# Performance work log

Measured on AMD Instinct MI355X. Metric: run time of the kernel, lower is better.

Reference implementation:

```python
import jax, jax.numpy as jnp
import numpy as np


def mish(x):
    return x * jnp.tanh(jax.nn.softplus(x))


def gcn(x, W, b, src, dst):
    # PyG GCNConv: h = D^-1/2 (A+I) D^-1/2 (x W) + b, aggregation at dst=edge_index[1]
    n = x.shape[0]
    h = x @ W
    deg = jax.ops.segment_sum(jnp.ones(src.shape[0], x.dtype), dst, num_segments=n) + 1.0
    dinv = jax.lax.rsqrt(deg)
    msg = h[src] * (dinv[src] * dinv[dst])[:, None]
    agg = jax.ops.segment_sum(msg, dst, num_segments=n)
    return agg + h * (dinv * dinv)[:, None] + b


def pool_mean(x, seg, num_segments):
    s = jax.ops.segment_sum(x, seg, num_segments=num_segments)
    c = jax.ops.segment_sum(jnp.ones(x.shape[0], x.dtype), seg, num_segments=num_segments)
    return s / jnp.maximum(c, 1.0)[:, None]


def attention(x, qW, qb, kW, kb, vW, vb, G):
    # x: [G*R, in_feats] -> per-graph self-attention over ROIs (dropout is identity in eval)
    R = x.shape[0] // G
    xc = x.reshape(G, R, x.shape[1])
    Q = xc @ qW + qb
    K = xc @ kW + kb
    Vv = xc @ vW + vb
    scores = jnp.einsum('gqd,gkd->gqk', Q, K) / (Q.shape[-1] ** 0.5)
    w = jax.nn.softmax(scores, axis=-1)
    out = jnp.einsum('gqk,gkd->gqd', w, Vv).reshape(G * R, Vv.shape[-1])
    return out, w.mean(axis=0)


def closs(a, b, temp=0.6):
    a = a / jnp.maximum(jnp.linalg.norm(a, axis=1, keepdims=True), 1e-12)
    b = b / jnp.maximum(jnp.linalg.norm(b, axis=1, keepdims=True), 1e-12)
    logits = (a @ b.T) / temp
    return -jnp.mean(jnp.diagonal(jax.nn.log_softmax(logits, axis=1)))


def setup_inputs() -> dict:
    key = jax.random.key(0)
    G, R1, R2, F_IN, H, OUT, DEG, V = 512, 200, 160, 128, 64, 64, 16, 64
    N1, N2 = G * R1, G * R2
    ks = iter(jax.random.split(key, 64))
    d = {}
    d['x1'] = jax.random.normal(next(ks), (N1, R1 + 3), jnp.float32)
    d['x2'] = jax.random.normal(next(ks), (N2, R2 + 3), jnp.float32)

    def lin(name, i, o):
        d[name + '_W'] = jax.random.normal(next(ks), (i, o), jnp.float32) * (i ** -0.5)
        d[name + '_b'] = jnp.zeros((o,), jnp.float32)

    lin('fcl', R1 + 3, F_IN); lin('fcr', R2 + 3, F_IN)
    lin('fcl1', R1, F_IN); lin('fcr1', R2, F_IN)
    lin('a1_q', F_IN, OUT); lin('a1_k', F_IN, OUT); lin('a1_v', F_IN, OUT)
    lin('a2_q', F_IN, OUT); lin('a2_k', F_IN, OUT); lin('a2_v', F_IN, OUT)
    lin('conv', F_IN, H); lin('conv1', H, H)
    lin('mlp', H, OUT)
    lin('fc1a', OUT * 4, F_IN); lin('fc1b', F_IN, 2)

    def edges(k, R):
        k1, k2 = jax.random.split(k)
        off = (jnp.arange(G, dtype=jnp.int32) * R)[:, None]
        src = jax.random.randint(k1, (G, R * DEG), 0, R, jnp.int32) + off
        dst = jax.random.randint(k2, (G, R * DEG), 0, R, jnp.int32) + off
        return jnp.stack([src.reshape(-1), dst.reshape(-1)])

    d['edge_index1'] = edges(next(ks), R1)
    d['edge_index2'] = edges(next(ks), R2)
    d['batch1'] = jnp.repeat(jnp.arange(G, dtype=jnp.int32), R1)
    d['batch2'] = jnp.repeat(jnp.arange(G, dtype=jnp.int32), R2)

    def sub(k, R):
        # one visited-node set (as in RW_subgraph) tiled per graph with offsets
        vis = jnp.sort(jax.random.permutation(k, R)[:V]).astype(jnp.int32)
        return (vis[None, :] + (jnp.arange(G, dtype=jnp.int32) * R)[:, None]).reshape(-1)

    d['sub_idx1'] = sub(next(ks), R1)
    d['sub_idx2'] = sub(next(ks), R2)
    d['num_graphs'] = G
    return d


def reference(x1, x2, fcl_W, fcl_b, fcr_W, fcr_b, fcl1_W, fcl1_b, fcr1_W, fcr1_b,
              a1_q_W, a1_q_b, a1_k_W, a1_k_b, a1_v_W, a1_v_b,
              a2_q_W, a2_q_b, a2_k_W, a2_k_b, a2_v_W, a2_v_b,
              conv_W, conv_b, conv1_W, conv1_b, mlp_W, mlp_b,
              fc1a_W, fc1a_b, fc1b_W, fc1b_b,
              edge_index1, edge_index2, batch1, batch2, sub_idx1, sub_idx2, num_graphs):
    G = int(num_graphs)
    src1, dst1 = edge_index1[0], edge_index1[1]
    src2, dst2 = edge_index2[0], edge_index2[1]

    z1 = x1[:, :-3] @ fcl1_W + fcl1_b
    z2 = x2[:, :-3] @ fcr1_W + fcr1_b
    z1, aw1 = attention(z1, a1_q_W, a1_q_b, a1_k_W, a1_k_b, a1_v_W, a1_v_b, G)
    z2, aw2 = attention(z2, a2_q_W, a2_q_b, a2_k_W, a2_k_b, a2_v_W, a2_v_b, G)
    z1 = pool_mean(z1, batch1, G)
    z2 = pool_mean(z2, batch2, G)

    h1 = x1 @ fcl_W + fcl_b
    h2 = x2 @ fcr_W + fcr_b
    o1 = mish(gcn(h1, conv_W, conv_b, src1, dst1))
    o2 = mish(gcn(h2, conv_W, conv_b, src2, dst2))
    o1 = gcn(o1, conv1_W, conv1_b, src1, dst1)
    o2 = gcn(o2, conv1_W, conv1_b, src2, dst2)

    s1 = o1[sub_idx1] @ mlp_W + mlp_b
    s2 = o2[sub_idx2] @ mlp_W + mlp_b
    s1 = pool_mean(s1, batch1[sub_idx1], G)
    s2 = pool_mean(s2, batch2[sub_idx2], G)

    c_loss = closs(s1, z2) + closs(z1, s2)
    feat = jnp.concatenate([s1, z1, s2, z2], axis=1)
    out = mish(feat @ fc1a_W + fc1a_b) @ fc1b_W + fc1b_b
    return c_loss, out, aw1, aw2
```

## Files before the change

### kernel.cpp

```cpp
#include <hip/hip_runtime.h>
#include <math.h>

#define TPB 256
#define MAXR 200
#define MAXEP 4608

typedef float f32x4 __attribute__((ext_vector_type(4)));
typedef __bf16 bfv8 __attribute__((ext_vector_type(8)));

union U8 { uint4 q; unsigned short us[8]; __bf16 b[8]; bfv8 v; };

__device__ __forceinline__ unsigned short f2bfu(float f) {
  union { __bf16 h; unsigned short u; } x;
  x.h = (__bf16)f;
  return x.u;
}
__device__ __forceinline__ float bfu2f(unsigned short u) {
  return __uint_as_float((unsigned)u << 16);
}

__device__ __forceinline__ float mish_f(float x) {
  float sp = fmaxf(x, 0.f) + log1pf(expf(-fabsf(x)));
  return x * tanhf(sp);
}

__device__ __forceinline__ U8 loadA_f32(const float* Af, int kb, int K, bool rowok) {
  U8 u;
  if (rowok && kb + 8 <= K) {
    float4 f0 = *(const float4*)(Af + kb);
    float4 f1 = *(const float4*)(Af + kb + 4);
    u.b[0]=(__bf16)f0.x; u.b[1]=(__bf16)f0.y; u.b[2]=(__bf16)f0.z; u.b[3]=(__bf16)f0.w;
    u.b[4]=(__bf16)f1.x; u.b[5]=(__bf16)f1.y; u.b[6]=(__bf16)f1.z; u.b[7]=(__bf16)f1.w;
  } else {
#pragma unroll
    for (int j = 0; j < 8; ++j) {
      float f = (rowok && kb + j < K) ? Af[kb + j] : 0.f;
      u.b[j] = (__bf16)f;
    }
  }
  return u;
}

template<bool ABF16, bool CBF16, int NJ, int KPMAX>
__global__ __launch_bounds__(256) void gemm2(
    const void* __restrict__ Av, const unsigned short* __restrict__ Bt,
    const float* __restrict__ bias, void* __restrict__ Cv,
    int N, int M, int K, int lda, int ldc,
    long sA, long sB, long sC, float alpha, int Kpad)
{
  constexpr int BM = NJ * 16;
  __shared__ unsigned short Bs[BM * KPMAX];

  const int tid = threadIdx.x;
  const int col0 = blockIdx.x * BM, row0 = blockIdx.y * 64;

  {
    const unsigned short* Bp = Bt + (long)blockIdx.z * sB + (long)col0 * Kpad;
    int rows = M - col0; if (rows > BM) rows = BM;
    const int total = rows * Kpad;
    for (int i = tid * 8; i < total; i += TPB * 32) {
      uint4 a0, a1, a2, a3;
      bool b1 = i + TPB * 8  < total;
      bool b2 = i + TPB * 16 < total;
      bool b3 = i + TPB * 24 < total;
      a0 = *(const uint4*)&Bp[i];
      if (b1) a1 = *(const uint4*)&Bp[i + TPB * 8];
      if (b2) a2 = *(const uint4*)&Bp[i + TPB * 16];
      if (b3) a3 = *(const uint4*)&Bp[i + TPB * 24];
      *(uint4*)&Bs[i] = a0;
      if (b1) *(uint4*)&Bs[i + TPB * 8]  = a1;
      if (b2) *(uint4*)&Bs[i + TPB * 16] = a2;
      if (b3) *(uint4*)&Bs[i + TPB * 24] = a3;
    }
  }

  const int lane = tid & 63, w = tid >> 6;
  const int mrow = lane & 15, kg = lane >> 4;
  const int arow = row0 + w * 16 + mrow;
  const bool rowok = arow < N;

  const unsigned short* Ah = nullptr;
  const float* Af = nullptr;
  if (ABF16) Ah = (const unsigned short*)Av + (long)blockIdx.z * sA + (long)arow * lda;
  else       Af = (const float*)Av + (long)blockIdx.z * sA + (long)arow * lda;

  U8 ua;
  if (ABF16) ua.q = *(const uint4*)(Ah + kg * 8);
  else       ua   = loadA_f32(Af, kg * 8, K, rowok);

  __syncthreads();

  f32x4 acc[NJ];
#pragma unroll
  for (int j = 0; j < NJ; ++j) acc[j] = (f32x4)0.f;

  for (int k0 = 0; k0 < K; k0 += 32) {
    U8 un;
    bool more = (k0 + 32) < K;
    if (more) {
      if (ABF16) un.q = *(const uint4*)(Ah + k0 + 32 + kg * 8);
      else       un   = loadA_f32(Af, k0 + 32 + kg * 8, K, rowok);
    }
    const int kb = k0 + kg * 8;
#pragma unroll
    for (int j = 0; j < NJ; ++j) {
      U8 ub;
      ub.q = *(const uint4*)&Bs[(j * 16 + mrow) * Kpad + kb];
      acc[j] = __builtin_amdgcn_mfma_f32_16x16x32_bf16(ua.v, ub.v, acc[j], 0, 0, 0);
    }
    if (more) ua = un;
  }

  long cbase = (long)blockIdx.z * sC;
#pragma unroll
  for (int j = 0; j < NJ; ++j) {
    int gc = col0 + j * 16 + mrow;
    if (gc >= M) continue;
    float bb = bias ? bias[gc] : 0.f;
#pragma unroll
    for (int r = 0; r < 4; ++r) {
      int gr = row0 + w * 16 + kg * 4 + r;
      if (gr >= N) continue;
      float v = acc[j][r] * alpha + bb;
      if (CBF16) ((unsigned short*)Cv)[cbase + (long)gr * ldc + gc] = f2bfu(v);
      else       ((float*)Cv)[cbase + (long)gr * ldc + gc] = v;
    }
  }
}

static inline int kpad_of(int K) { return ((K + 31) / 32) * 32 + 8; }

struct PrepSeg { const float* src; void* dst; int K, M, Kpad, kind; };
struct PrepArgs { PrepSeg s[19]; };

__global__ __launch_bounds__(256) void prep_weights(PrepArgs a) {
  PrepSeg sg = a.s[blockIdx.x];
  if (sg.kind == 0) {
    unsigned short* d = (unsigned short*)sg.dst;
    int tot = sg.M * sg.Kpad;
    for (int i = threadIdx.x; i < tot; i += TPB) {
      int m = i / sg.Kpad, k = i - m * sg.Kpad;
      float f = (k < sg.K) ? sg.src[(long)k * sg.M + m] : 0.f;
      d[i] = f2bfu(f);
    }
  } else {
    float* d = (float*)sg.dst;
    for (int i = threadIdx.x; i < sg.K; i += TPB) d[i] = sg.src[i];
  }
}

__global__ __launch_bounds__(256) void xcast(const float* __restrict__ x,
                                             unsigned short* __restrict__ xb,
                                             int C, int S)
{
  long r0 = (long)blockIdx.x * 8;
  for (int i = threadIdx.x; i < 8 * S; i += TPB) {
    int rr = i / S, c = i - rr * S;
    long r = r0 + rr;
    xb[r * S + c] = f2bfu(c < C ? x[r * C + c] : 0.f);
  }
}

__global__ __launch_bounds__(256) void ktvt_kernel(
    const unsigned short* __restrict__ QKV, unsigned short* __restrict__ Kt,
    unsigned short* __restrict__ Vt, int R, int Rpad)
{
  int g = blockIdx.x;
  const unsigned short* q = QKV + (long)g * R * 192;
  unsigned short* kt = Kt + (long)g * R * 72;
  unsigned short* vt = Vt + (long)g * 64 * Rpad;
  int c = threadIdx.x & 63, w = threadIdx.x >> 6;
  for (int r = w; r < R; r += 4) {
    kt[r * 72 + c] = q[(long)r * 192 + 64 + c];
    vt[c * Rpad + r] = q[(long)r * 192 + 128 + c];
  }
  int pad = Rpad - R;
  for (int i = threadIdx.x; i < 64 * pad; i += TPB) {
    int cc = i / pad, k = i - cc * pad;
    vt[cc * Rpad + R + k] = 0;
  }
}

__global__ __launch_bounds__(256) void gcn_kernel(
    const unsigned short* __restrict__ hWb, const int* __restrict__ src,
    const int* __restrict__ dst, const float* __restrict__ bias,
    unsigned short* __restrict__ outb, int R, int EPG, int do_mish)
{
  __shared__ unsigned short hWs[(MAXR + 1) * 64];
  __shared__ float dinv_s[MAXR];
  __shared__ unsigned short ssrc[MAXEP];
  __shared__ int cnt[256];
  __shared__ int scan[256];
  __shared__ int offx[257];
  __shared__ int cur[256];

  int g = blockIdx.x, tid = threadIdx.x;
  long base = (long)g * R * 64;
  long ebase = (long)g * EPG;
  int gR = g * R;
  int RF = R * 64;

  cnt[tid] = 0;
  __syncthreads();
  for (int e = tid; e < EPG; e += TPB)
    atomicAdd(&cnt[dst[ebase + e] - gR], 1);
  __syncthreads();

  int x = cnt[tid];
  int pc = (x + 7) & ~7;
  scan[tid] = pc;
  __syncthreads();
#pragma unroll
  for (int s = 1; s < 256; s <<= 1) {
    int t = (tid >= s) ? scan[tid - s] : 0;
    __syncthreads();
    scan[tid] += t;
    __syncthreads();
  }
  if (tid == 0) offx[0] = 0;
  offx[tid + 1] = scan[tid];
  cur[tid] = scan[tid] - pc;
  if (tid < R) dinv_s[tid] = rsqrtf((float)x + 1.f);
  {
    unsigned dummy2 = (unsigned)R | ((unsigned)R << 16);
    for (int i = tid; i < MAXEP / 2; i += TPB) ((unsigned*)ssrc)[i] = dummy2;
  }
  __syncthreads();

  for (int e = tid; e < EPG; e += TPB) {
    int d = dst[ebase + e] - gR;
    int s = src[ebase + e] - gR;
    int pos = atomicAdd(&cur[d], 1);
    ssrc[pos] = (unsigned short)s;
  }
  for (int i = tid * 8; i < RF; i += TPB * 8) {
    U8 u; u.q = *(const uint4*)&hWb[base + i];
    float di = dinv_s[i >> 6];
#pragma unroll
    for (int j = 0; j < 8; ++j) u.us[j] = f2bfu(bfu2f(u.us[j]) * di);
    *(uint4*)&hWs[i] = u.q;
  }
  if (tid < 64) hWs[(R << 6) | tid] = 0;
  __syncthreads();

  int lane = tid & 63, w = tid >> 6;
  for (int d = w; d < R; d += 4) {
    int i = offx[d], eEnd = offx[d + 1];
    float acc = 0.f;
    for (; i < eEnd; i += 8) {
      U8 u; u.q = *(const uint4*)&ssrc[i];
      float a0 = bfu2f(hWs[((int)u.us[0] << 6) | lane]);
      float a1 = bfu2f(hWs[((int)u.us[1] << 6) | lane]);
      float a2 = bfu2f(hWs[((int)u.us[2] << 6) | lane]);
      float a3 = bfu2f(hWs[((int)u.us[3] << 6) | lane]);
      float a4 = bfu2f(hWs[((int)u.us[4] << 6) | lane]);
      float a5 = bfu2f(hWs[((int)u.us[5] << 6) | lane]);
      float a6 = bfu2f(hWs[((int)u.us[6] << 6) | lane]);
      float a7 = bfu2f(hWs[((int)u.us[7] << 6) | lane]);
      acc += ((a0 + a1) + (a2 + a3)) + ((a4 + a5) + (a6 + a7));
    }
    float di = dinv_s[d];
    float v = di * (acc + bfu2f(hWs[(d << 6) | lane])) + bias[lane];
    if (do_mish) v = mish_f(v);
    outb[base + ((long)d << 6) + lane] = f2bfu(v);
  }
}

__global__ __launch_bounds__(256) void softmax_bf16(unsigned short* __restrict__ S,
                                                    int R, long rows)
{
  long wid = (long)blockIdx.x * 4 + (threadIdx.x >> 6);
  if (wid >= rows) return;
  int lane = threadIdx.x & 63;
  unsigned short* row = S + wid * R;
  float v[4];
  float mx = -1e30f;
#pragma unroll
  for (int t = 0; t < 4; ++t) {
    int j = lane + t * 64;
    v[t] = (j < R) ? bfu2f(row[j]) : -1e30f;
    mx = fmaxf(mx, v[t]);
  }
#pragma unroll
  for (int o = 32; o; o >>= 1) mx = fmaxf(mx, __shfl_xor(mx, o));
  float s = 0.f;
#pragma unroll
  for (int t = 0; t < 4; ++t) {
    int j = lane + t * 64;
    if (j < R) { v[t] = expf(v[t] - mx); s += v[t]; }
  }
#pragma unroll
  for (int o = 32; o; o >>= 1) s += __shfl_xor(s, o);
  float inv = 1.f / s;
#pragma unroll
  for (int t = 0; t < 4; ++t) {
    int j = lane + t * 64;
    if (j < R) row[j] = f2bfu(v[t] * inv);
  }
}

__global__ void meang_bf16(const unsigned short* __restrict__ S, float* __restrict__ out,
                           int RR, int G, float inv)
{
  int idx = blockIdx.x * TPB + threadIdx.x;
  if (idx >= RR) return;
  const unsigned short* p = S + idx;
  float s = 0.f;
  for (int g = 0; g + 8 <= G; g += 8) {
    s += bfu2f(p[(long)g * RR])       + bfu2f(p[(long)(g + 1) * RR]) +
         bfu2f(p[(long)(g + 2) * RR]) + bfu2f(p[(long)(g + 3) * RR]) +
         bfu2f(p[(long)(g + 4) * RR]) + bfu2f(p[(long)(g + 5) * RR]) +
         bfu2f(p[(long)(g + 6) * RR]) + bfu2f(p[(long)(g + 7) * RR]);
  }
  out[idx] = s * inv;
}

__global__ __launch_bounds__(64) void pool_mean_kernel(const float* __restrict__ X,
                                                       float* __restrict__ out, int R)
{
  int g = blockIdx.x, lane = threadIdx.x;
  const float* p = X + (long)g * R * 64 + lane;
  float s = 0.f;
  for (int r = 0; r + 4 <= R; r += 4)
    s += p[(long)r * 64] + p[(long)(r + 1) * 64] + p[(long)(r + 2) * 64] + p[(long)(r + 3) * 64];
  out[g * 64 + lane] = s * (1.f / R);
}

__global__ __launch_bounds__(64) void sub_mean_kernel(const unsigned short* __restrict__ X,
                                                      const int* __restrict__ sub,
                                                      float* __restrict__ out, int V)
{
  int g = blockIdx.x, lane = threadIdx.x;
  float s = 0.f;
  for (int v = 0; v + 4 <= V; v += 4) {
    int i0 = sub[g * V + v],     i1 = sub[g * V + v + 1];
    int i2 = sub[g * V + v + 2], i3 = sub[g * V + v + 3];
    s += bfu2f(X[(long)i0 * 64 + lane]) + bfu2f(X[(long)i1 * 64 + lane]) +
         bfu2f(X[(long)i2 * 64 + lane]) + bfu2f(X[(long)i3 * 64 + lane]);
  }
  out[g * 64 + lane] = s * (1.f / V);
}

__global__ __launch_bounds__(64) void norm_rows_kernel(const float* __restrict__ X,
                                                       float* __restrict__ Y)
{
  int g = blockIdx.x, lane = threadIdx.x;
  float x = X[g * 64 + lane];
  float ss = x * x;
#pragma unroll
  for (int o = 32; o; o >>= 1) ss += __shfl_xor(ss, o);
  float n = fmaxf(sqrtf(ss), 1e-12f);
  Y[g * 64 + lane] = x / n;
}

__global__ __launch_bounds__(256) void closs_kernel(const float* __restrict__ An,
                                                    const float* __restrict__ Bn,
                                                    float* __restrict__ loss, int G,
                                                    float invTemp, float coef)
{
  int i = blockIdx.x;
  __shared__ float arow[64];
  __shared__ float logits[512];
  __shared__ float red[256];
  int t = threadIdx.x;
  if (t < 64) arow[t] = An[i * 64 + t];
  __syncthreads();
  for (int j = t; j < G; j += 256) {
    const float* bp = Bn + (long)j * 64;
    float d = 0.f;
#pragma unroll
    for (int k = 0; k < 64; ++k) d = fmaf(arow[k], bp[k], d);
    logits[j] = d * invTemp;
  }
  __syncthreads();
  float mx = -1e30f;
  for (int j = t; j < G; j += 256) mx = fmaxf(mx, logits[j]);
  red[t] = mx; __syncthreads();
  for (int o = 128; o; o >>= 1) { if (t < o) red[t] = fmaxf(red[t], red[t + o]); __syncthreads(); }
  mx = red[0]; __syncthreads();
  float s = 0.f;
  for (int j = t; j < G; j += 256) s += expf(logits[j] - mx);
  red[t] = s; __syncthreads();
  for (int o = 128; o; o >>= 1) { if (t < o) red[t] += red[t + o]; __syncthreads(); }
  if (t == 0) {
    float lse = mx + logf(red[0]);
    atomicAdd(loss, coef * (lse - logits[i]));
  }
}

__global__ __launch_bounds__(128) void head_kernel(
    const float* __restrict__ s1, const float* __restrict__ z1,
    const float* __restrict__ s2, const float* __restrict__ z2,
    const float* __restrict__ W1, const float* __restrict__ b1,
    const float* __restrict__ W2, const float* __restrict__ b2,
    float* __restrict__ out)
{
  int g = blockIdx.x, t = threadIdx.x;
  __shared__ float feat[256];
  __shared__ float hid[128];
  if (t < 64) {
    feat[t]       = s1[g * 64 + t];
    feat[64 + t]  = z1[g * 64 + t];
    feat[128 + t] = s2[g * 64 + t];
    feat[192 + t] = z2[g * 64 + t];
  }
  __syncthreads();
  float acc = b1[t];
  for (int k = 0; k < 256; ++k) acc = fmaf(feat[k], W1[k * 128 + t], acc);
  hid[t] = mish_f(acc);
  __syncthreads();
  if (t < 2) {
    float a2 = b2[t];
#pragma unroll
    for (int k = 0; k < 128; ++k) a2 = fmaf(hid[k], W2[k * 2 + t], a2);
    out[g * 2 + t] = a2;
  }
}

#define LAUNCH_GEMM(ABF,CBF,NJ,KP, A,B,BI,C, N,M,K,LDA,LDC,SA,SB,SC,BAT,AL,KPAD) \
  { dim3 g_(((M)+(NJ)*16-1)/((NJ)*16), ((N)+63)/64, (BAT)); \
    gemm2<ABF,CBF,NJ,KP><<<g_,256,0,stream>>>((A),(B),(BI),(C),(N),(M),(K),(LDA),(LDC),(SA),(SB),(SC),(AL),(KPAD)); }

extern "C" void kernel_launch(void* const* d_in, const int* in_sizes, int n_in,
                              void* d_out, int out_size, void* d_ws, size_t ws_size,
                              hipStream_t stream)
{
  const float* x1     = (const float*)d_in[0];
  const float* x2     = (const float*)d_in[1];
  const float* fcl_W  = (const float*)d_in[2];  const float* fcl_b  = (const float*)d_in[3];
  const float* fcr_W  = (const float*)d_in[4];  const float* fcr_b  = (const float*)d_in[5];
  const float* fcl1_W = (const float*)d_in[6];  const float* fcl1_b = (const float*)d_in[7];
  const float* fcr1_W = (const float*)d_in[8];  const float* fcr1_b = (const float*)d_in[9];
  const float* a1qW = (const float*)d_in[10]; const float* a1qb = (const float*)d_in[11];
  const float* a1kW = (const float*)d_in[12]; const float* a1kb = (const float*)d_in[13];
  const float* a1vW = (const float*)d_in[14]; const float* a1vb = (const float*)d_in[15];
  const float* a2qW = (const float*)d_in[16]; const float* a2qb = (const float*)d_in[17];
  const float* a2kW = (const float*)d_in[18]; const float* a2kb = (const float*)d_in[19];
  const float* a2vW = (const float*)d_in[20]; const float* a2vb = (const float*)d_in[21];
  const float* convW  = (const float*)d_in[22]; const float* convb  = (const float*)d_in[23];
  const float* conv1W = (const float*)d_in[24]; const float* conv1b = (const float*)d_in[25];
  const float* mlpW   = (const float*)d_in[26]; const float* mlpb   = (const float*)d_in[27];
  const float* fc1aW  = (const float*)d_in[28]; const float* fc1ab  = (const float*)d_in[29];
  const float* fc1bW  = (const float*)d_in[30]; const float* fc1bb  = (const float*)d_in[31];
  const int* ei1  = (const int*)d_in[32];
  const int* ei2  = (const int*)d_in[33];
  const int* sub1 = (const int*)d_in[36];
  const int* sub2 = (const int*)d_in[37];

  const int R1 = in_sizes[6] / 128;
  const int R2 = in_sizes[8] / 128;
  const int N1 = in_sizes[34];
  const int N2 = in_sizes[35];
  const int G  = N1 / R1;
  const int E1 = in_sizes[32] / 2, E2 = in_sizes[33] / 2;
  const int EPG1 = E1 / G, EPG2 = E2 / G;
  const int V = in_sizes[36] / G;

  const int XS = 232;
  const int Kp1  = kpad_of(R1);
  const int Kp2  = kpad_of(R2);
  const int Kp1f = kpad_of(R1 + 3);
  const int Kp2f = kpad_of(R2 + 3);
  const int Rpad1 = Kp1, Rpad2 = Kp2;

  char* wp = (char*)d_ws;
  auto alloc = [&](size_t bytes) -> char* {
    char* p = wp; wp += (bytes + 255) & ~(size_t)255; return p;
  };
  unsigned short* x1b = (unsigned short*)alloc((size_t)N1 * XS * 2);
  unsigned short* x2b = (unsigned short*)alloc((size_t)N2 * XS * 2);
  size_t raSh = (size_t)G * R1 * R1;
  if ((size_t)N1 * 128 > raSh) raSh = (size_t)N1 * 128;
  unsigned short* RA = (unsigned short*)alloc(raSh * 2);
  unsigned short* RB = (unsigned short*)alloc((size_t)N1 * 192 * 2);
  unsigned short* Kt = (unsigned short*)alloc((size_t)G * R1 * 72 * 2);
  unsigned short* Vt = (unsigned short*)alloc((size_t)G * 64 * Rpad1 * 2);
  float* W5 = (float*)alloc((size_t)N1 * 64 * 4);
  unsigned short* fcl1t  = (unsigned short*)alloc((size_t)128 * Kp1 * 2);
  unsigned short* fcr1t  = (unsigned short*)alloc((size_t)128 * Kp2 * 2);
  unsigned short* fclt   = (unsigned short*)alloc((size_t)128 * Kp1f * 2);
  unsigned short* fcrt   = (unsigned short*)alloc((size_t)128 * Kp2f * 2);
  unsigned short* Wc1t   = (unsigned short*)alloc((size_t)192 * 136 * 2);
  unsigned short* Wc2t   = (unsigned short*)alloc((size_t)192 * 136 * 2);
  unsigned short* convt  = (unsigned short*)alloc((size_t)64 * 136 * 2);
  unsigned short* conv1t = (unsigned short*)alloc((size_t)64 * 72 * 2);
  unsigned short* mlpt   = (unsigned short*)alloc((size_t)64 * 72 * 2);
  float* bc1 = (float*)alloc(192 * 4);
  float* bc2 = (float*)alloc(192 * 4);
  float* Pz1 = (float*)alloc((size_t)G * 64 * 4);
  float* Pz2 = (float*)alloc((size_t)G * 64 * 4);
  float* Ps1 = (float*)alloc((size_t)G * 64 * 4);
  float* Ps2 = (float*)alloc((size_t)G * 64 * 4);
  float* Mt  = (float*)alloc((size_t)G * 64 * 4);
  float* n_s1 = (float*)alloc((size_t)G * 64 * 4);
  float* n_z2 = (float*)alloc((size_t)G * 64 * 4);
  float* n_z1 = (float*)alloc((size_t)G * 64 * 4);
  float* n_s2 = (float*)alloc((size_t)G * 64 * 4);
  (void)alloc(4096);

  float* loss = (float*)d_out;
  float* outp = loss + 1;
  float* aw1  = outp + (size_t)G * 2;
  float* aw2  = aw1 + (size_t)R1 * R1;

  hipMemsetAsync(d_out, 0, sizeof(float), stream);

  PrepArgs pa;
  int seg = 0;
  auto addp = [&](const float* s, unsigned short* d, int K, int M, int Kp) {
    pa.s[seg].src = s; pa.s[seg].dst = d; pa.s[seg].K = K; pa.s[seg].M = M;
    pa.s[seg].Kpad = Kp; pa.s[seg].kind = 0; seg++;
  };
  auto addb = [&](const float* s, float* d, int n) {
    pa.s[seg].src = s; pa.s[seg].dst = d; pa.s[seg].K = n; pa.s[seg].M = 0;
    pa.s[seg].Kpad = 0; pa.s[seg].kind = 1; seg++;
  };
  addp(fcl1_W, fcl1t, R1, 128, Kp1);
  addp(fcr1_W, fcr1t, R2, 128, Kp2);
  addp(fcl_W,  fclt,  R1 + 3, 128, Kp1f);
  addp(fcr_W,  fcrt,  R2 + 3, 128, Kp2f);
  addp(a1qW, Wc1t,             128, 64, 136);
  addp(a1kW, Wc1t + 64 * 136,  128, 64, 136);
  addp(a1vW, Wc1t + 128 * 136, 128, 64, 136);
  addp(a2qW, Wc2t,             128, 64, 136);
  addp(a2kW, Wc2t + 64 * 136,  128, 64, 136);
  addp(a2vW, Wc2t + 128 * 136, 128, 64, 136);
  addp(convW,  convt,  128, 64, 136);
  addp(conv1W, conv1t, 64, 64, 72);
  addp(mlpW,   mlpt,   64, 64, 72);
  addb(a1qb, bc1, 64); addb(a1kb, bc1 + 64, 64); addb(a1vb, bc1 + 128, 64);
  addb(a2qb, bc2, 64); addb(a2kb, bc2 + 64, 64); addb(a2vb, bc2 + 128, 64);
  prep_weights<<<seg, 256, 0, stream>>>(pa);

  xcast<<<N1 / 8, 256, 0, stream>>>(x1, x1b, R1 + 3, XS);
  xcast<<<N2 / 8, 256, 0, stream>>>(x2, x2b, R2 + 3, XS);

  LAUNCH_GEMM(true, true, 8, 232, x1b, fcl1t, fcl1_b, RA,
              N1, 128, R1, XS, 128, 0, 0, 0, 1, 1.f, Kp1);
  LAUNCH_GEMM(true, true, 12, 136, RA, Wc1t, bc1, RB,
              N1, 192, 128, 128, 192, 0, 0, 0, 1, 1.f, 136);
  ktvt_kernel<<<G, 256, 0, stream>>>(RB, Kt, Vt, R1, Rpad1);
  LAUNCH_GEMM(true, true, 8, 72, RB, Kt, nullptr, RA,
              R1, R1, 64, 192, R1, (long)R1 * 192, (long)R1 * 72, (long)R1 * R1,
              G, 0.125f, 72);
  {
    long rows = (long)G * R1;
    softmax_bf16<<<(int)((rows + 3) / 4), 256, 0, stream>>>(RA, R1, rows);
    meang_bf16<<<(R1 * R1 + TPB - 1) / TPB, TPB, 0, stream>>>(RA, aw1, R1 * R1, G, 1.f / G);
  }
  LAUNCH_GEMM(true, false, 4, 232, RA, Vt, nullptr, W5,
              R1, 64, R1, R1, 64, (long)R1 * R1, (long)64 * Rpad1, (long)R1 * 64,
              G, 1.f, Rpad1);
  pool_mean_kernel<<<G, 64, 0, stream>>>(W5, Pz1, R1);

  LAUNCH_GEMM(true, true, 8, 232, x2b, fcr1t, fcr1_b, RA,
              N2, 128, R2, XS, 128, 0, 0, 0, 1, 1.f, Kp2);
  LAUNCH_GEMM(true, true, 12, 136, RA, Wc2t, bc2, RB,
              N2, 192, 128, 128, 192, 0, 0, 0, 1, 1.f, 136);
  ktvt_kernel<<<G, 256, 0, stream>>>(RB, Kt, Vt, R2, Rpad2);
  LAUNCH_GEMM(true, true, 8, 72, RB, Kt, nullptr, RA,
              R2, R2, 64, 192, R2, (long)R2 * 192, (long)R2 * 72, (long)R2 * R2,
              G, 0.125f, 72);
  {
    long rows = (long)G * R2;
    softmax_bf16<<<(int)((rows + 3) / 4), 256, 0, stream>>>(RA, R2, rows);
    meang_bf16<<<(R2 * R2 + TPB - 1) / TPB, TPB, 0, stream>>>(RA, aw2, R2 * R2, G, 1.f / G);
  }
  LAUNCH_GEMM(true, false, 4, 232, RA, Vt, nullptr, W5,
              R2, 64, R2, R2, 64, (long)R2 * R2, (long)64 * Rpad2, (long)R2 * 64,
              G, 1.f, Rpad2);
  pool_mean_kernel<<<G, 64, 0, stream>>>(W5, Pz2, R2);

  unsigned short* hW0 = RB;
  unsigned short* hW1 = RB + (size_t)N1 * 64;
  unsigned short* hW2 = RB + (size_t)N1 * 128;
  LAUNCH_GEMM(true, true, 8, 232, x1b, fclt, fcl_b, RA,
              N1, 128, R1 + 3, XS, 128, 0, 0, 0, 1, 1.f, Kp1f);
  LAUNCH_GEMM(true, true, 4, 136, RA, convt, nullptr, hW0,
              N1, 64, 128, 128, 64, 0, 0, 0, 1, 1.f, 136);
  gcn_kernel<<<G, 256, 0, stream>>>(hW0, ei1, ei1 + E1, convb, hW1, R1, EPG1, 1);
  LAUNCH_GEMM(true, true, 4, 136, hW1, conv1t, nullptr, hW2,
              N1, 64, 64, 64, 64, 0, 0, 0, 1, 1.f, 72);
  gcn_kernel<<<G, 256, 0, stream>>>(hW2, ei1, ei1 + E1, conv1b, hW0, R1, EPG1, 0);
  sub_mean_kernel<<<G, 64, 0, stream>>>(hW0, sub1, Mt, V);
  LAUNCH_GEMM(false, false, 4, 136, Mt, mlpt, mlpb, Ps1,
              G, 64, 64, 64, 64, 0, 0, 0, 1, 1.f, 72);

  LAUNCH_GEMM(true, true, 8, 232, x2b, fcrt, fcr_b, RA,
              N2, 128, R2 + 3, XS, 128, 0, 0, 0, 1, 1.f, Kp2f);
  LAUNCH_GEMM(true, true, 4, 136, RA, convt, nullptr, hW0,
              N2, 64, 128, 128, 64, 0, 0, 0, 1, 1.f, 136);
  gcn_kernel<<<G, 256, 0, stream>>>(hW0, ei2, ei2 + E2, convb, hW1, R2, EPG2, 1);
  LAUNCH_GEMM(true, true, 4, 136, hW1, conv1t, nullptr, hW2,
              N2, 64, 64, 64, 64, 0, 0, 0, 1, 1.f, 72);
  gcn_kernel<<<G, 256, 0, stream>>>(hW2, ei2, ei2 + E2, conv1b, hW0, R2, EPG2, 0);
  sub_mean_kernel<<<G, 64, 0, stream>>>(hW0, sub2, Mt, V);
  LAUNCH_GEMM(false, false, 4, 136, Mt, mlpt, mlpb, Ps2,
              G, 64, 64, 64, 64, 0, 0, 0, 1, 1.f, 72);

  norm_rows_kernel<<<G, 64, 0, stream>>>(Ps1, n_s1);
  norm_rows_kernel<<<G, 64, 0, stream>>>(Pz2, n_z2);
  norm_rows_kernel<<<G, 64, 0, stream>>>(Pz1, n_z1);
  norm_rows_kernel<<<G, 64, 0, stream>>>(Ps2, n_s2);
  const float invTemp = 1.f / 0.6f;
  closs_kernel<<<G, 256, 0, stream>>>(n_s1, n_z2, loss, G, invTemp, 1.f / G);
  closs_kernel<<<G, 256, 0, stream>>>(n_z1, n_s2, loss, G, invTemp, 1.f / G);

  head_kernel<<<G, 128, 0, stream>>>(Ps1, Pz1, Ps2, Pz2, fc1aW, fc1ab, fc1bW, fc1bb, outp);
}
```

Baseline: 941.5 us.

## Replace sparse GCN aggregation with dense per-graph normalized adjacency MFMA GEMM

Each graph's normalized adjacency (with self-loops and D^-1/2 scaling) is built once as a dense bf16 matrix, and GCN aggregation becomes a batched MFMA GEMM against the transposed features, with bias and mish fused into the GEMM epilogue. The attention output is also written as bf16, and pool_mean switches to a 256-thread bf16 reduction. This swaps LDS gather aggregation for tensor-core dense work, at the cost of extra adjacency-build and transpose kernels and O(R^2) dense FLOPs on a sparse graph. The adjacency is stored in bf16 and overwrites the x buffers, which adds rounding error.

```diff
diff --git a/kernel.cpp b/kernel.cpp
--- a/kernel.cpp
+++ b/kernel.cpp
@@ -41,7 +41,7 @@
   return u;
 }
 
-template<bool ABF16, bool CBF16, int NJ, int KPMAX>
+template<bool ABF16, bool CBF16, bool MISH, int NJ, int KPMAX>
 __global__ __launch_bounds__(256) void gemm2(
     const void* __restrict__ Av, const unsigned short* __restrict__ Bt,
     const float* __restrict__ bias, void* __restrict__ Cv,
@@ -122,6 +122,7 @@
       int gr = row0 + w * 16 + kg * 4 + r;
       if (gr >= N) continue;
       float v = acc[j][r] * alpha + bb;
+      if (MISH) v = mish_f(v);
       if (CBF16) ((unsigned short*)Cv)[cbase + (long)gr * ldc + gc] = f2bfu(v);
       else       ((float*)Cv)[cbase + (long)gr * ldc + gc] = v;
     }
@@ -181,24 +182,21 @@
   }
 }
 
-__global__ __launch_bounds__(256) void gcn_kernel(
-    const unsigned short* __restrict__ hWb, const int* __restrict__ src,
-    const int* __restrict__ dst, const float* __restrict__ bias,
-    unsigned short* __restrict__ outb, int R, int EPG, int do_mish)
-{
-  __shared__ unsigned short hWs[(MAXR + 1) * 64];
-  __shared__ float dinv_s[MAXR];
+__global__ __launch_bounds__(256) void adj_build(
+    const int* __restrict__ src, const int* __restrict__ dst,
+    unsigned short* __restrict__ Adj, int R, int Rpad, int EPG)
+{
+  __shared__ float dinv_s[256];
   __shared__ unsigned short ssrc[MAXEP];
   __shared__ int cnt[256];
   __shared__ int scan[256];
   __shared__ int offx[257];
   __shared__ int cur[256];
+  __shared__ float rowbuf[4][256];
 
   int g = blockIdx.x, tid = threadIdx.x;
-  long base = (long)g * R * 64;
   long ebase = (long)g * EPG;
   int gR = g * R;
-  int RF = R * 64;
 
   cnt[tid] = 0;
   __syncthreads();
@@ -220,9 +218,9 @@
   if (tid == 0) offx[0] = 0;
   offx[tid + 1] = scan[tid];
   cur[tid] = scan[tid] - pc;
-  if (tid < R) dinv_s[tid] = rsqrtf((float)x + 1.f);
+  dinv_s[tid] = rsqrtf((float)x + 1.f);
   {
-    unsigned dummy2 = (unsigned)R | ((unsigned)R << 16);
+    unsigned dummy2 = 0xFFFFFFFFu;
     for (int i = tid; i < MAXEP / 2; i += TPB) ((unsigned*)ssrc)[i] = dummy2;
   }
   __syncthreads();
@@ -233,36 +231,55 @@
     int pos = atomicAdd(&cur[d], 1);
     ssrc[pos] = (unsigned short)s;
   }
-  for (int i = tid * 8; i < RF; i += TPB * 8) {
-    U8 u; u.q = *(const uint4*)&hWb[base + i];
-    float di = dinv_s[i >> 6];
-#pragma unroll
-    for (int j = 0; j < 8; ++j) u.us[j] = f2bfu(bfu2f(u.us[j]) * di);
-    *(uint4*)&hWs[i] = u.q;
-  }
-  if (tid < 64) hWs[(R << 6) | tid] = 0;
   __syncthreads();
 
   int lane = tid & 63, w = tid >> 6;
+  float* rb = rowbuf[w];
   for (int d = w; d < R; d += 4) {
-    int i = offx[d], eEnd = offx[d + 1];
-    float acc = 0.f;
-    for (; i < eEnd; i += 8) {
-      U8 u; u.q = *(const uint4*)&ssrc[i];
-      float a0 = bfu2f(hWs[((int)u.us[0] << 6) | lane]);
-      float a1 = bfu2f(hWs[((int)u.us[1] << 6) | lane]);
-      float a2 = bfu2f(hWs[((int)u.us[2] << 6) | lane]);
-      float a3 = bfu2f(hWs[((int)u.us[3] << 6) | lane]);
-      float a4 = bfu2f(hWs[((int)u.us[4] << 6) | lane]);
-      float a5 = bfu2f(hWs[((int)u.us[5] << 6) | lane]);
-      float a6 = bfu2f(hWs[((int)u.us[6] << 6) | lane]);
-      float a7 = bfu2f(hWs[((int)u.us[7] << 6) | lane]);
-      acc += ((a0 + a1) + (a2 + a3)) + ((a4 + a5) + (a6 + a7));
-    }
-    float di = dinv_s[d];
-    float v = di * (acc + bfu2f(hWs[(d << 6) | lane])) + bias[lane];
-    if (do_mish) v = mish_f(v);
-    outb[base + ((long)d << 6) + lane] = f2bfu(v);
+#pragma unroll
+    for (int i = 0; i < 4; ++i) rb[lane + i * 64] = 0.f;
+    int i0 = offx[d], i1 = offx[d + 1];
+    for (int i = i0 + lane; i < i1; i += 64) {
+      int s = ssrc[i];
+      if (s < R) atomicAdd(&rb[s], dinv_s[s]);
+    }
+    float dd = dinv_s[d];
+    int c0 = lane * 4;
+    if (c0 < Rpad) {
+      ushort4 o;
+      float v0 = rb[c0]     + (c0     == d ? dd : 0.f);
+      float v1 = rb[c0 + 1] + (c0 + 1 == d ? dd : 0.f);
+      float v2 = rb[c0 + 2] + (c0 + 2 == d ? dd : 0.f);
+      float v3 = rb[c0 + 3] + (c0 + 3 == d ? dd : 0.f);
+      o.x = f2bfu(v0 * dd); o.y = f2bfu(v1 * dd);
+      o.z = f2bfu(v2 * dd); o.w = f2bfu(v3 * dd);
+      *(ushort4*)&Adj[((long)gR + d) * Rpad + c0] = o;
+    }
+  }
+}
+
+__global__ __launch_bounds__(256) void transp64(
+    const unsigned short* __restrict__ X, unsigned short* __restrict__ XT,
+    int R, int Rpad)
+{
+  __shared__ unsigned short tile[64][72];
+  int g = blockIdx.x, tid = threadIdx.x;
+  const unsigned short* xg = X + (long)g * R * 64;
+  unsigned short* xt = XT + (long)g * 64 * Rpad;
+  for (int r0 = 0; r0 < Rpad; r0 += 64) {
+    __syncthreads();
+    for (int i = tid; i < 64 * 64; i += TPB) {
+      int rr = i >> 6, cc = i & 63;
+      int r = r0 + rr;
+      tile[cc][rr] = (r < R) ? xg[(long)r * 64 + cc] : (unsigned short)0;
+    }
+    __syncthreads();
+    int c = tid >> 2, j0 = (tid & 3) * 16;
+    int lim = Rpad - r0; if (lim > 64) lim = 64;
+    for (int jj = j0; jj < j0 + 16 && jj < lim; jj += 8) {
+      uint4 q = *(const uint4*)&tile[c][jj];
+      *(uint4*)&xt[(long)c * Rpad + r0 + jj] = q;
+    }
   }
 }
 
@@ -315,15 +332,18 @@
   out[idx] = s * inv;
 }
 
-__global__ __launch_bounds__(64) void pool_mean_kernel(const float* __restrict__ X,
-                                                       float* __restrict__ out, int R)
-{
-  int g = blockIdx.x, lane = threadIdx.x;
-  const float* p = X + (long)g * R * 64 + lane;
+__global__ __launch_bounds__(256) void pool_mean_bf16(const unsigned short* __restrict__ X,
+                                                      float* __restrict__ out, int R)
+{
+  __shared__ float part[4][64];
+  int g = blockIdx.x, lane = threadIdx.x & 63, w = threadIdx.x >> 6;
   float s = 0.f;
-  for (int r = 0; r + 4 <= R; r += 4)
-    s += p[(long)r * 64] + p[(long)(r + 1) * 64] + p[(long)(r + 2) * 64] + p[(long)(r + 3) * 64];
-  out[g * 64 + lane] = s * (1.f / R);
+  for (int r = w; r < R; r += 4)
+    s += bfu2f(X[((long)g * R + r) * 64 + lane]);
+  part[w][lane] = s;
+  __syncthreads();
+  if (w == 0)
+    out[g * 64 + lane] = (part[0][lane] + part[1][lane] + part[2][lane] + part[3][lane]) * (1.f / R);
 }
 
 __global__ __launch_bounds__(64) void sub_mean_kernel(const unsigned short* __restrict__ X,
@@ -417,9 +437,9 @@
   }
 }
 
-#define LAUNCH_GEMM(ABF,CBF,NJ,KP, A,B,BI,C, N,M,K,LDA,LDC,SA,SB,SC,BAT,AL,KPAD) \
+#define LAUNCH_GEMM(ABF,CBF,MISH,NJ,KP, A,B,BI,C, N,M,K,LDA,LDC,SA,SB,SC,BAT,AL,KPAD) \
   { dim3 g_(((M)+(NJ)*16-1)/((NJ)*16), ((N)+63)/64, (BAT)); \
-    gemm2<ABF,CBF,NJ,KP><<<g_,256,0,stream>>>((A),(B),(BI),(C),(N),(M),(K),(LDA),(LDC),(SA),(SB),(SC),(AL),(KPAD)); }
+    gemm2<ABF,CBF,MISH,NJ,KP><<<g_,256,0,stream>>>((A),(B),(BI),(C),(N),(M),(K),(LDA),(LDC),(SA),(SB),(SC),(AL),(KPAD)); }
 
 extern "C" void kernel_launch(void* const* d_in, const int* in_sizes, int n_in,
                               void* d_out, int out_size, void* d_ws, size_t ws_size,
@@ -475,7 +495,7 @@
   unsigned short* RB = (unsigned short*)alloc((size_t)N1 * 192 * 2);
   unsigned short* Kt = (unsigned short*)alloc((size_t)G * R1 * 72 * 2);
   unsigned short* Vt = (unsigned short*)alloc((size_t)G * 64 * Rpad1 * 2);
-  float* W5 = (float*)alloc((size_t)N1 * 64 * 4);
+  unsigned short* W5 = (unsigned short*)alloc((size_t)N1 * 64 * 2);
   unsigned short* fcl1t  = (unsigned short*)alloc((size_t)128 * Kp1 * 2);
   unsigned short* fcr1t  = (unsigned short*)alloc((size_t)128 * Kp2 * 2);
   unsigned short* fclt   = (unsigned short*)alloc((size_t)128 * Kp1f * 2);
@@ -497,6 +517,9 @@
   float* n_z1 = (float*)alloc((size_t)G * 64 * 4);
   float* n_s2 = (float*)alloc((size_t)G * 64 * 4);
   (void)alloc(4096);
+
+  unsigned short* Adj1 = x1b;
+  unsigned short* Adj2 = x2b;
 
   float* loss = (float*)d_out;
   float* outp = loss + 1;
@@ -535,12 +558,12 @@
   xcast<<<N1 / 8, 256, 0, stream>>>(x1, x1b, R1 + 3, XS);
   xcast<<<N2 / 8, 256, 0, stream>>>(x2, x2b, R2 + 3, XS);
 
-  LAUNCH_GEMM(true, true, 8, 232, x1b, fcl1t, fcl1_b, RA,
+  LAUNCH_GEMM(true, true, false, 8, 232, x1b, fcl1t, fcl1_b, RA,
               N1, 128, R1, XS, 128, 0, 0, 0, 1, 1.f, Kp1);
-  LAUNCH_GEMM(true, true, 12, 136, RA, Wc1t, bc1, RB,
+  LAUNCH_GEMM(true, true, false, 12, 136, RA, Wc1t, bc1, RB,
               N1, 192, 128, 128, 192, 0, 0, 0, 1, 1.f, 136);
   ktvt_kernel<<<G, 256, 0, stream>>>(RB, Kt, Vt, R1, Rpad1);
-  LAUNCH_GEMM(true, true, 8, 72, RB, Kt, nullptr, RA,
+  LAUNCH_GEMM(true, true, false, 8, 72, RB, Kt, nullptr, RA,
               R1, R1, 64, 192, R1, (long)R1 * 192, (long)R1 * 72, (long)R1 * R1,
               G, 0.125f, 72);
   {
@@ -548,17 +571,17 @@
     softmax_bf16<<<(int)((rows + 3) / 4), 256, 0, stream>>>(RA, R1, rows);
     meang_bf16<<<(R1 * R1 + TPB - 1) / TPB, TPB, 0, stream>>>(RA, aw1, R1 * R1, G, 1.f / G);
   }
-  LAUNCH_GEMM(true, false, 4, 232, RA, Vt, nullptr, W5,
+  LAUNCH_GEMM(true, true, false, 4, 232, RA, Vt, nullptr, W5,
               R1, 64, R1, R1, 64, (long)R1 * R1, (long)64 * Rpad1, (long)R1 * 64,
               G, 1.f, Rpad1);
-  pool_mean_kernel<<<G, 64, 0, stream>>>(W5, Pz1, R1);
-
-  LAUNCH_GEMM(true, true, 8, 232, x2b, fcr1t, fcr1_b, RA,
+  pool_mean_bf16<<<G, 256, 0, stream>>>(W5, Pz1, R1);
+
+  LAUNCH_GEMM(true, true, false, 8, 232, x2b, fcr1t, fcr1_b, RA,
               N2, 128, R2, XS, 128, 0, 0, 0, 1, 1.f, Kp2);
-  LAUNCH_GEMM(true, true, 12, 136, RA, Wc2t, bc2, RB,
+  LAUNCH_GEMM(true, true, false, 12, 136, RA, Wc2t, bc2, RB,
               N2, 192, 128, 128, 192, 0, 0, 0, 1, 1.f, 136);
   ktvt_kernel<<<G, 256, 0, stream>>>(RB, Kt, Vt, R2, Rpad2);
-  LAUNCH_GEMM(true, true, 8, 72, RB, Kt, nullptr, RA,
+  LAUNCH_GEMM(true, true, false, 8, 72, RB, Kt, nullptr, RA,
               R2, R2, 64, 192, R2, (long)R2 * 192, (long)R2 * 72, (long)R2 * R2,
               G, 0.125f, 72);
   {
@@ -566,36 +589,50 @@
     softmax_bf16<<<(int)((rows + 3) / 4), 256, 0, stream>>>(RA, R2, rows);
     meang_bf16<<<(R2 * R2 + TPB - 1) / TPB, TPB, 0, stream>>>(RA, aw2, R2 * R2, G, 1.f / G);
   }
-  LAUNCH_GEMM(true, false, 4, 232, RA, Vt, nullptr, W5,
+  LAUNCH_GEMM(true, true, false, 4, 232, RA, Vt, nullptr, W5,
               R2, 64, R2, R2, 64, (long)R2 * R2, (long)64 * Rpad2, (long)R2 * 64,
               G, 1.f, Rpad2);
-  pool_mean_kernel<<<G, 64, 0, stream>>>(W5, Pz2, R2);
+  pool_mean_bf16<<<G, 256, 0, stream>>>(W5, Pz2, R2);
 
   unsigned short* hW0 = RB;
   unsigned short* hW1 = RB + (size_t)N1 * 64;
   unsigned short* hW2 = RB + (size_t)N1 * 128;
-  LAUNCH_GEMM(true, true, 8, 232, x1b, fclt, fcl_b, RA,
+  LAUNCH_GEMM(true, true, false, 8, 232, x1b, fclt, fcl_b, RA,
               N1, 128, R1 + 3, XS, 128, 0, 0, 0, 1, 1.f, Kp1f);
-  LAUNCH_GEMM(true, true, 4, 136, RA, convt, nullptr, hW0,
+  LAUNCH_GEMM(true, true, false, 4, 136, RA, convt, nullptr, hW0,
               N1, 64, 128, 128, 64, 0, 0, 0, 1, 1.f, 136);
-  gcn_kernel<<<G, 256, 0, stream>>>(hW0, ei1, ei1 + E1, convb, hW1, R1, EPG1, 1);
-  LAUNCH_GEMM(true, true, 4, 136, hW1, conv1t, nullptr, hW2,
+  adj_build<<<G, 256, 0, stream>>>(ei1, ei1 + E1, Adj1, R1, Rpad1, EPG1);
+  transp64<<<G, 256, 0, stream>>>(hW0, Vt, R1, Rpad1);
+  LAUNCH_GEMM(true, true, true, 4, 232, Adj1, Vt, convb, hW1,
+              R1, 64, R1, Rpad1, 64, (long)R1 * Rpad1, (long)64 * Rpad1, (long)R1 * 64,
+              G, 1.f, Rpad1);
+  LAUNCH_GEMM(true, true, false, 4, 136, hW1, conv1t, nullptr, hW2,
               N1, 64, 64, 64, 64, 0, 0, 0, 1, 1.f, 72);
-  gcn_kernel<<<G, 256, 0, stream>>>(hW2, ei1, ei1 + E1, conv1b, hW0, R1, EPG1, 0);
+  transp64<<<G, 256, 0, stream>>>(hW2, Vt, R1, Rpad1);
+  LAUNCH_GEMM(true, true, false, 4, 232, Adj1, Vt, conv1b, hW0,
+              R1, 64, R1, Rpad1, 64, (long)R1 * Rpad1, (long)64 * Rpad1, (long)R1 * 64,
+              G, 1.f, Rpad1);
   sub_mean_kernel<<<G, 64, 0, stream>>>(hW0, sub1, Mt, V);
-  LAUNCH_GEMM(false, false, 4, 136, Mt, mlpt, mlpb, Ps1,
+  LAUNCH_GEMM(false, false, false, 4, 136, Mt, mlpt, mlpb, Ps1,
               G, 64, 64, 64, 64, 0, 0, 0, 1, 1.f, 72);
 
-  LAUNCH_GEMM(true, true, 8, 232, x2b, fcrt, fcr_b, RA,
+  LAUNCH_GEMM(true, true, false, 8, 232, x2b, fcrt, fcr_b, RA,
               N2, 128, R2 + 3, XS, 128, 0, 0, 0, 1, 1.f, Kp2f);
-  LAUNCH_GEMM(true, true, 4, 136, RA, convt, nullptr, hW0,
+  LAUNCH_GEMM(true, true, false, 4, 136, RA, convt, nullptr, hW0,
               N2, 64, 128, 128, 64, 0, 0, 0, 1, 1.f, 136);
-  gcn_kernel<<<G, 256, 0, stream>>>(hW0, ei2, ei2 + E2, convb, hW1, R2, EPG2, 1);
-  LAUNCH_GEMM(true, true, 4, 136, hW1, conv1t, nullptr, hW2,
+  adj_build<<<G, 256, 0, stream>>>(ei2, ei2 + E2, Adj2, R2, Rpad2, EPG2);
+  transp64<<<G, 256, 0, stream>>>(hW0, Vt, R2, Rpad2);
+  LAUNCH_GEMM(true, true, true, 4, 232, Adj2, Vt, convb, hW1,
+              R2, 64, R2, Rpad2, 64, (long)R2 * Rpad2, (long)64 * Rpad2, (long)R2 * 64,
+              G, 1.f, Rpad2);
+  LAUNCH_GEMM(true, true, false, 4, 136, hW1, conv1t, nullptr, hW2,
               N2, 64, 64, 64, 64, 0, 0, 0, 1, 1.f, 72);
-  gcn_kernel<<<G, 256, 0, stream>>>(hW2, ei2, ei2 + E2, conv1b, hW0, R2, EPG2, 0);
+  transp64<<<G, 256, 0, stream>>>(hW2, Vt, R2, Rpad2);
+  LAUNCH_GEMM(true, true, false, 4, 232, Adj2, Vt, conv1b, hW0,
+              R2, 64, R2, Rpad2, 64, (long)R2 * Rpad2, (long)64 * Rpad2, (long)R2 * 64,
+              G, 1.f, Rpad2);
   sub_mean_kernel<<<G, 64, 0, stream>>>(hW0, sub2, Mt, V);
-  LAUNCH_GEMM(false, false, 4, 136, Mt, mlpt, mlpb, Ps2,
+  LAUNCH_GEMM(false, false, false, 4, 136, Mt, mlpt, mlpb, Ps2,
               G, 64, 64, 64, 64, 0, 0, 0, 1, 1.f, 72);
 
   norm_rows_kernel<<<G, 64, 0, stream>>>(Ps1, n_s1);
```

Measured after the change: 1.007 ms. 7.0% more time.
